# Kernel optimization log

Measured on AMD Instinct MI355X. Metric: run time of the kernel, lower is better.

The kernel has to match this reference:

```python
import jax, jax.numpy as jnp
import numpy as np

B, SEQ, D, INITIAL_D, T_DIFF = 256, 200, 256, 256, 1000


def _linear_params(key, fan_in, fan_out):
    k1, k2 = jax.random.split(key)
    lim = 1.0 / np.sqrt(fan_in)
    w = jax.random.uniform(k1, (fan_in, fan_out), minval=-lim, maxval=lim, dtype=jnp.float32)
    b = jax.random.uniform(k2, (fan_out,), minval=-lim, maxval=lim, dtype=jnp.float32)
    return w, b


def setup_inputs() -> dict:
    key = jax.random.key(0)
    ks = list(jax.random.split(key, 24))
    inp = {}
    inp["input_seqs"] = jax.random.normal(ks[0], (B, SEQ, INITIAL_D), dtype=jnp.float32)
    inp["masks"] = jnp.zeros((B, SEQ), dtype=jnp.int32)
    inp["lengths"] = jnp.full((B,), SEQ, dtype=jnp.int32)
    inp["seq_time_step"] = jax.random.uniform(ks[1], (B, SEQ), dtype=jnp.float32) * 360.0
    inp["code_masks"] = jnp.zeros((B, SEQ), dtype=jnp.int32)
    inp["diffusion_time_t"] = jax.random.randint(ks[2], (B,), 0, T_DIFF)
    inp["normal_noise"] = jax.random.normal(ks[3], (B, SEQ, D), dtype=jnp.float32)
    inp["predicted_noise"] = jax.random.normal(ks[4], (B, SEQ, D), dtype=jnp.float32) * 0.1
    inp["betas"] = jnp.linspace(1e-4, 0.02, T_DIFF, dtype=jnp.float32)
    names = [("emb2", INITIAL_D, D), ("Wall", D, 4 * D), ("Uall", D, 4 * D), ("Wd", D, D),
             ("time", 64, D), ("sel", 1, 64), ("whk", D, D), ("w1", 2 * D, 64),
             ("w2", 64, 2), ("out", D, 2)]
    for i, (nm, fi, fo) in enumerate(names):
        w, b = _linear_params(ks[5 + i], fi, fo)
        inp[nm + "_w"] = w
        inp[nm + "_b"] = b
    return inp


def reference(input_seqs, masks, lengths, seq_time_step, code_masks,
              diffusion_time_t, normal_noise, predicted_noise, betas,
              emb2_w, emb2_b, Wall_w, Wall_b, Uall_w, Uall_b, Wd_w, Wd_b,
              time_w, time_b, sel_w, sel_b, whk_w, whk_b,
              w1_w, w1_b, w2_w, w2_b, out_w, out_b):
    x = input_seqs @ emb2_w + emb2_b                      # [b,seq,d]  (initial_d != 0 path)
    b, seq, d = x.shape
    t = seq_time_step[..., None] / 180.0                  # [b,seq,1]
    tfeat = 1.0 - jnp.tanh(jnp.square(t @ sel_w + sel_b))  # [b,seq,64]
    time_feature = tfeat @ time_w + time_b                # [b,seq,d]

    def tlstm(xs_tmajor, tf_tmajor):
        # xs_tmajor, tf_tmajor: [seq, b, d] -> hidden states [b, seq, d]
        def step(carry, inp):
            h, c = carry
            xs, ts = inp
            c_s1 = jnp.tanh(c @ Wd_w + Wd_b)
            c_adj = c - c_s1 + c_s1 * ts                  # time-decayed cell
            gates = jax.nn.sigmoid(h @ Wall_w + Wall_b + xs @ Uall_w + Uall_b)
            f, i, o, ct = jnp.split(gates, 4, axis=-1)    # note: c_tmp uses sigmoid too
            c_new = f * c_adj + i * ct
            h_new = o * jnp.tanh(c_new)
            return (h_new, c_new), h_new
        zeros = jnp.zeros((xs_tmajor.shape[1], d), xs_tmajor.dtype)
        _, hs = jax.lax.scan(step, (zeros, zeros), (xs_tmajor, tf_tmajor))
        return hs.transpose(1, 0, 2)                      # [b,seq,d]

    tf_t = time_feature.transpose(1, 0, 2)
    outputs = tlstm(x.transpose(1, 0, 2), tf_t)

    # attention alignment (original always uses e_k = x[:, 0:1]) — fully vectorized over i>=1
    e_k = x[:, :1, :]                                     # [b,1,d]
    whk = outputs[:, :-1, :] @ whk_w + whk_b              # [b,seq-1,d]
    cat = jnp.concatenate([jnp.broadcast_to(e_k, whk.shape), whk], axis=-1)
    attn = jax.nn.softmax(jnp.tanh(cat @ w1_w + w1_b) @ w2_w + w2_b, axis=-1)  # [b,seq-1,2]
    aligned = jnp.concatenate([e_k, e_k * attn[..., 0:1] + whk * attn[..., 1:2]], axis=1)

    alpha = jnp.cumprod(1.0 - betas)[diffusion_time_t].reshape(-1, 1, 1)
    _noisy = aligned * jnp.sqrt(alpha) + normal_noise * jnp.sqrt(1.0 - alpha)  # UNet input (UNet output stubbed as predicted_noise)
    gen_x = aligned + (normal_noise - predicted_noise)
    gen_outputs = tlstm(gen_x.transpose(1, 0, 2), tf_t)

    out = jnp.max(outputs, axis=1) @ out_w + out_b        # max-pool over seq, then mlp
    gen_out = jnp.max(gen_outputs, axis=1) @ out_w + out_b
    return (out, gen_out, predicted_noise, normal_noise)
```

## Files before the change

### kernel.cpp

```cpp
#include <hip/hip_runtime.h>
#include <hip/hip_bf16.h>
#include <cstdint>

typedef __attribute__((ext_vector_type(8))) short short8;
typedef __attribute__((ext_vector_type(4))) float f32x4;
typedef unsigned short ushortT;

#define SEQ 200
#define NB  256

__device__ __forceinline__ float b2f(ushortT u){
    union { unsigned u; float f; } v; v.u = ((unsigned)u) << 16; return v.f;
}
__device__ __forceinline__ ushortT f2b(float f){
    union { float f; unsigned u; } v; v.f = f;
    unsigned r = v.u + 0x7FFFu + ((v.u >> 16) & 1u);
    return (ushortT)(r >> 16);
}
__device__ __forceinline__ float frcp(float x){
    float r; asm("v_rcp_f32 %0, %1" : "=v"(r) : "v"(x)); return r;
}
__device__ __forceinline__ float sigm(float x){ return frcp(1.0f + __expf(-x)); }
__device__ __forceinline__ float tanh_fast(float x){
    float ax = fabsf(x);
    float t = __expf(-2.0f * ax);
    float r = (1.0f - t) * frcp(1.0f + t);
    return copysignf(r, x);
}

__global__ void k_cvt(const float* __restrict__ in, ushortT* __restrict__ out){
    size_t i = ((size_t)blockIdx.x*256 + threadIdx.x)*4;
    float4 v = *(const float4*)(in + i);
    ushortT o[4] = { f2b(v.x), f2b(v.y), f2b(v.z), f2b(v.w) };
    *(int2*)(out + i) = *(int2*)o;
}

__global__ void k_swizzle(const float* __restrict__ src, int ncols,
                          ushortT* __restrict__ dst, int tile0){
    int Tl = blockIdx.x, q = blockIdx.y, l = threadIdx.x;
    int n  = Tl*16 + (l & 15);
    int kb = q*32 + (l >> 4)*8;
    short8 v;
    #pragma unroll
    for (int j = 0; j < 8; ++j) ((ushortT*)&v)[j] = f2b(src[(size_t)(kb + j)*ncols + n]);
    *(short8*)(dst + ((size_t)(tile0 + Tl)*8 + q)*512 + (size_t)l*8) = v;
}

__global__ void k_tft(const float* __restrict__ sts, const float* __restrict__ selw,
                      const float* __restrict__ selb, ushortT* __restrict__ tft){
    int l = threadIdx.x, g = blockIdx.x / SEQ, t = blockIdx.x % SEQ;
    int lm = l & 15, lq = l >> 4;
    float tv = sts[(size_t)(g*16 + lm)*SEQ + t] * (1.0f/180.0f);
    size_t base = (size_t)(g*SEQ + t)*1024 + (size_t)l*8;
    #pragma unroll
    for (int q = 0; q < 2; ++q){
        short8 v;
        #pragma unroll
        for (int j = 0; j < 8; ++j){
            int u = q*32 + lq*8 + j;
            float a = tv * selw[u] + selb[u];
            ((ushortT*)&v)[j] = f2b(1.0f - tanh_fast(a*a));
        }
        *(short8*)(tft + base + (size_t)q*512) = v;
    }
}

__global__ __launch_bounds__(512) void k_gemm256(const ushortT* A,
        const ushortT* __restrict__ Bswz, const float* __restrict__ bias, ushortT* out){
    __shared__ ushortT stage[16*256];
    int tid = threadIdx.x, w = tid >> 6, l = tid & 63, lm = l & 15, lq = l >> 4;
    size_t r0 = (size_t)blockIdx.x * 16;
    const f32x4 fz = {0.f,0.f,0.f,0.f};
    f32x4 acc[2] = {fz, fz};
    for (int q = 0; q < 8; ++q){
        short8 a = *(const short8*)(A + (r0 + lm)*256 + q*32 + lq*8);
        #pragma unroll
        for (int p = 0; p < 2; ++p){
            int T = 2*w + p;
            short8 b = *(const short8*)(Bswz + ((size_t)T*8 + q)*512 + (size_t)l*8);
            acc[p] = __builtin_amdgcn_mfma_f32_16x16x32_bf16(a, b, acc[p], 0, 0, 0);
        }
    }
    #pragma unroll
    for (int p = 0; p < 2; ++p){
        int n = (2*w + p)*16 + lm;
        float bs = bias[n];
        #pragma unroll
        for (int r = 0; r < 4; ++r)
            stage[(lq*4 + r)*256 + n] = f2b(acc[p][r] + bs);
    }
    __syncthreads();
    int row = tid >> 5, c8 = tid & 31;
    int4 v = *(const int4*)(stage + row*256 + c8*8);
    *(int4*)(out + (r0 + row)*256 + (size_t)c8*8) = v;
}

__global__ __launch_bounds__(256) void k_gemm64(const ushortT* __restrict__ A,
        const ushortT* __restrict__ Bswz, float* __restrict__ out){
    int tid = threadIdx.x, w = tid >> 6, l = tid & 63, lm = l & 15, lq = l >> 4;
    size_t r0 = (size_t)blockIdx.x * 16;
    const f32x4 fz = {0.f,0.f,0.f,0.f};
    f32x4 acc = fz;
    for (int q = 0; q < 8; ++q){
        short8 a = *(const short8*)(A + (r0 + lm)*256 + q*32 + lq*8);
        short8 b = *(const short8*)(Bswz + ((size_t)w*8 + q)*512 + (size_t)l*8);
        acc = __builtin_amdgcn_mfma_f32_16x16x32_bf16(a, b, acc, 0, 0, 0);
    }
    #pragma unroll
    for (int r = 0; r < 4; ++r)
        out[(r0 + lq*4 + r)*64 + w*16 + lm] = acc[r];
}

__global__ __launch_bounds__(512) void k_gemmgates(const ushortT* __restrict__ A,
        const ushortT* __restrict__ Bswz, const float* __restrict__ bW,
        const float* __restrict__ bU, ushortT* __restrict__ out){
    int tid = threadIdx.x, w = tid >> 6, l = tid & 63, lm = l & 15, lq = l >> 4;
    int g = blockIdx.x / SEQ, t = blockIdx.x % SEQ;
    const f32x4 fz = {0.f,0.f,0.f,0.f};
    f32x4 acc[8] = {fz,fz,fz,fz,fz,fz,fz,fz};
    const ushortT* Arow = A + ((size_t)(g*16 + lm)*SEQ + t)*256;
    for (int q = 0; q < 8; ++q){
        short8 a = *(const short8*)(Arow + q*32 + lq*8);
        #pragma unroll
        for (int gq = 0; gq < 4; ++gq)
        #pragma unroll
        for (int p = 0; p < 2; ++p){
            int T = gq*16 + 2*w + p;
            short8 b = *(const short8*)(Bswz + ((size_t)T*8 + q)*512 + (size_t)l*8);
            acc[gq*2+p] = __builtin_amdgcn_mfma_f32_16x16x32_bf16(a, b, acc[gq*2+p], 0, 0, 0);
        }
    }
    short8 ch[4];
    #pragma unroll
    for (int gq = 0; gq < 4; ++gq)
    #pragma unroll
    for (int p = 0; p < 2; ++p){
        int n = gq*256 + w*32 + p*16 + lm;
        float bs = bW[n] + bU[n];
        #pragma unroll
        for (int r = 0; r < 4; ++r)
            ((ushortT*)&ch[p*2 + (gq>>1)])[(gq&1)*4 + r] = f2b(acc[gq*2+p][r] + bs);
    }
    size_t base = (size_t)(g*SEQ + t)*16384 + (size_t)(w*64 + l)*32;
    #pragma unroll
    for (int ci = 0; ci < 4; ++ci) *(short8*)(out + base + ci*8) = ch[ci];
}

__global__ void k_zeroflags(unsigned* __restrict__ f){
    f[blockIdx.x*256 + threadIdx.x] = 0;
}

#define HB (16*264)
__global__ __launch_bounds__(512, 2) void k_scan(const ushortT* __restrict__ xg,
        const ushortT* __restrict__ tftg, const ushortT* __restrict__ Wswz,
        const ushortT* __restrict__ twswz, const float* __restrict__ wdb_g,
        const float* __restrict__ timeb, ushortT* __restrict__ hs,
        float* __restrict__ maxh, int write_hs,
        ushortT* __restrict__ xbuf, unsigned* __restrict__ flags, unsigned fb){
    extern __shared__ ushortT smem[];
    ushortT* wlds = smem + 4*HB;
    int tid = threadIdx.x, w = tid >> 6, l = tid & 63, lm = l & 15, lq = l >> 4;
    int blk = blockIdx.x;
    int h = blk >> 4, g = blk & 15;
    int pblk = (1 - h)*16 + g;
    int cw = h*8 + w;
    int col = cw*16 + lm;
    int l8 = l*8;
    float wdb = wdb_g[col];
    float tb  = timeb[col];
    short8 twf[2];
    #pragma unroll
    for (int q2 = 0; q2 < 2; ++q2)
        twf[q2] = *(const short8*)(twswz + ((size_t)cw*8 + q2)*512 + l8);
    short8 wg0[8], wg1[8], wg2[8], wdreg[8];
    #pragma unroll
    for (int q = 0; q < 8; ++q){
        wg0[q]   = *(const short8*)(Wswz + ((size_t)( 0 + cw)*8 + q)*512 + l8);
        wg1[q]   = *(const short8*)(Wswz + ((size_t)(16 + cw)*8 + q)*512 + l8);
        wg2[q]   = *(const short8*)(Wswz + ((size_t)(32 + cw)*8 + q)*512 + l8);
        wdreg[q] = *(const short8*)(Wswz + ((size_t)(64 + cw)*8 + q)*512 + l8);
    }
    float c[4], hm[4];
    #pragma unroll
    for (int i = 0; i < 4; ++i){ c[i] = 0.0f; hm[i] = -2.0f; }
    for (int i = tid; i < HB; i += 512){ smem[HB + i] = 0; smem[3*HB + i] = 0; }
    {
        const int4* wsrc = (const int4*)(Wswz + (size_t)(48 + h*8)*4096);
        int4* wdst = (int4*)wlds;
        for (int i = tid; i < 4096; i += 512) wdst[i] = wsrc[i];
    }
    __syncthreads();

    const ushortT* xg_g  = xg   + (size_t)g*SEQ*16384 + ((size_t)(cw>>1)*64 + l)*32 + (cw&1)*16;
    const ushortT* tft_g = tftg + (size_t)g*SEQ*1024  + (size_t)l8;
    const ushortT* wl    = wlds + (size_t)w*4096 + l8;
    const f32x4 fz = {0.f,0.f,0.f,0.f};

    for (int t = 0; t < SEQ; ++t){
        int pb = t & 1, ab = 1 - pb;
        const ushortT* hb = smem + (size_t)ab*HB;
        const ushortT* cb = smem + 2*HB + (size_t)ab*HB;
        short8 xA  = *(const short8*)(xg_g + (size_t)t*16384);
        short8 xB  = *(const short8*)(xg_g + (size_t)t*16384 + 8);
        short8 aT0 = *(const short8*)(tft_g + (size_t)t*1024);
        short8 aT1 = *(const short8*)(tft_g + (size_t)t*1024 + 512);

        f32x4 acc[5];
        #pragma unroll
        for (int i = 0; i < 5; ++i) acc[i] = fz;
        #pragma unroll
        for (int q = 0; q < 8; ++q){
            short8 a  = *(const short8*)(hb + lm*264 + q*32 + lq*8);
            short8 ca = *(const short8*)(cb + lm*264 + q*32 + lq*8);
            short8 b3 = *(const short8*)(wl + q*512);
            acc[0] = __builtin_amdgcn_mfma_f32_16x16x32_bf16(a,  wg0[q],   acc[0], 0, 0, 0);
            acc[1] = __builtin_amdgcn_mfma_f32_16x16x32_bf16(a,  wg1[q],   acc[1], 0, 0, 0);
            acc[2] = __builtin_amdgcn_mfma_f32_16x16x32_bf16(a,  wg2[q],   acc[2], 0, 0, 0);
            acc[3] = __builtin_amdgcn_mfma_f32_16x16x32_bf16(a,  b3,       acc[3], 0, 0, 0);
            acc[4] = __builtin_amdgcn_mfma_f32_16x16x32_bf16(ca, wdreg[q], acc[4], 0, 0, 0);
        }
        f32x4 acc_ts = fz;
        acc_ts = __builtin_amdgcn_mfma_f32_16x16x32_bf16(aT0, twf[0], acc_ts, 0, 0, 0);
        acc_ts = __builtin_amdgcn_mfma_f32_16x16x32_bf16(aT1, twf[1], acc_ts, 0, 0, 0);

        ushortT* hbw = smem + (size_t)pb*HB;
        ushortT* cbw = smem + 2*HB + (size_t)pb*HB;
        #pragma unroll
        for (int r = 0; r < 4; ++r){
            float F   = acc[0][r] + b2f(((const ushortT*)&xA)[r]);
            float I   = acc[1][r] + b2f(((const ushortT*)&xA)[4+r]);
            float O   = acc[2][r] + b2f(((const ushortT*)&xB)[r]);
            float CT  = acc[3][r] + b2f(((const ushortT*)&xB)[4+r]);
            float cwd = acc[4][r] + wdb;
            float ts  = acc_ts[r] + tb;
            float cc  = c[r];
            float cs1 = tanh_fast(cwd);
            float cadj = cc - cs1 + cs1*ts;
            float cn  = sigm(F)*cadj + sigm(I)*sigm(CT);
            float hv  = sigm(O)*tanh_fast(cn);
            c[r]  = cn;
            hm[r] = fmaxf(hm[r], hv);
            hbw[(lq*4 + r)*264 + col] = f2b(hv);
            cbw[(lq*4 + r)*264 + col] = f2b(cn);
        }
        __syncthreads();
        if (t < SEQ-1){
            {
                int part = tid >> 8, i = tid & 255, row = i >> 4, c16 = i & 15;
                const ushortT* src = (part ? cbw : hbw) + row*264 + h*128 + c16*8;
                union { int4 v; unsigned long long uu[2]; } u; u.v = *(const int4*)src;
                unsigned long long* dst = (unsigned long long*)(xbuf +
                    ((((size_t)blk*2 + pb)*2 + part)*16 + row)*128 + c16*8);
                __hip_atomic_store(dst+0, u.uu[0], __ATOMIC_RELAXED, __HIP_MEMORY_SCOPE_AGENT);
                __hip_atomic_store(dst+1, u.uu[1], __ATOMIC_RELAXED, __HIP_MEMORY_SCOPE_AGENT);
            }
            __syncthreads();
            if (tid == 0){
                __hip_atomic_store(&flags[(size_t)blk*64], fb + (unsigned)t + 1u,
                                   __ATOMIC_RELEASE, __HIP_MEMORY_SCOPE_AGENT);
                unsigned want = fb + (unsigned)t + 1u;
                for (int it = 0; it < 20000000; ++it){
                    if (__hip_atomic_load(&flags[(size_t)pblk*64],
                            __ATOMIC_ACQUIRE, __HIP_MEMORY_SCOPE_AGENT) >= want) break;
                    __builtin_amdgcn_s_sleep(2);
                }
            }
            if (write_hs && tid >= 256){
                int i = tid - 256, row = i >> 4, c16 = i & 15;
                int4 v = *(const int4*)(hbw + row*264 + h*128 + c16*8);
                *(int4*)(hs + ((size_t)(g*16 + row)*SEQ + t)*256 + h*128 + c16*8) = v;
            }
            __syncthreads();
            {
                int part = tid >> 8, i = tid & 255, row = i >> 4, c16 = i & 15;
                const unsigned long long* src = (const unsigned long long*)(xbuf +
                    ((((size_t)pblk*2 + pb)*2 + part)*16 + row)*128 + c16*8);
                unsigned long long u0 = __hip_atomic_load(src+0, __ATOMIC_RELAXED, __HIP_MEMORY_SCOPE_AGENT);
                unsigned long long u1 = __hip_atomic_load(src+1, __ATOMIC_RELAXED, __HIP_MEMORY_SCOPE_AGENT);
                ushortT* dst = (part ? cbw : hbw) + row*264 + (1-h)*128 + c16*8;
                union { int4 v; unsigned long long uu[2]; } u;
                u.uu[0] = u0; u.uu[1] = u1;
                *(int4*)dst = u.v;
            }
            __syncthreads();
        } else {
            if (write_hs && tid < 256){
                int row = tid >> 4, c16 = tid & 15;
                int4 v = *(const int4*)(hbw + row*264 + h*128 + c16*8);
                *(int4*)(hs + ((size_t)(g*16 + row)*SEQ + t)*256 + h*128 + c16*8) = v;
            }
        }
    }
    #pragma unroll
    for (int r = 0; r < 4; ++r)
        maxh[(size_t)(g*16 + lq*4 + r)*256 + col] = hm[r];
}

__global__ void k_ekcopy(const ushortT* __restrict__ x, ushortT* __restrict__ ek){
    int b = blockIdx.x, l = threadIdx.x;
    ((int2*)(ek + (size_t)b*256))[l] = ((const int2*)(x + (size_t)b*SEQ*256))[l];
}

__global__ void k_ekw(const ushortT* __restrict__ ek, const float* __restrict__ w1w,
                      const float* __restrict__ w1b, float* __restrict__ ekw){
    int b = blockIdx.x, l = threadIdx.x;
    float acc = w1b[l];
    const ushortT* e = ek + (size_t)b*256;
    for (int d = 0; d < 256; ++d)
        acc += b2f(e[d]) * w1w[(size_t)d*64 + l];
    ekw[b*64 + l] = acc;
}

__global__ __launch_bounds__(512) void k_attn(const ushortT* __restrict__ ekbuf,
        const ushortT* __restrict__ whk, const float* __restrict__ ekw,
        const float* __restrict__ w1p, const float* __restrict__ w2w,
        const float* __restrict__ w2b, const float* __restrict__ nn,
        const float* __restrict__ pn, ushortT* __restrict__ genx){
    int w = threadIdx.x >> 6, l = threadIdx.x & 63;
    int wid = blockIdx.x*8 + w;
    int b = wid / SEQ, sp = wid % SEQ;
    const ushortT* ek = ekbuf + (size_t)b*256;
    const ushortT* wr = whk + ((size_t)b*SEQ + (sp > 0 ? sp-1 : 0))*256;
    size_t orow = ((size_t)b*SEQ + sp)*256;
    float a0, a1;
    if (sp == 0){ a0 = 1.0f; a1 = 0.0f; }
    else {
        float acc = ekw[b*64 + l] + w1p[((size_t)b*SEQ + sp-1)*64 + l];
        float u  = tanh_fast(acc);
        float p0 = u * w2w[l*2 + 0];
        float p1 = u * w2w[l*2 + 1];
        #pragma unroll
        for (int off = 32; off >= 1; off >>= 1){
            p0 += __shfl_xor(p0, off, 64);
            p1 += __shfl_xor(p1, off, 64);
        }
        float v0 = p0 + w2b[0], v1 = p1 + w2b[1];
        a0 = sigm(v0 - v1); a1 = 1.0f - a0;
    }
    #pragma unroll
    for (int i = 0; i < 4; ++i){
        int d = i*64 + l;
        float al = b2f(ek[d])*a0 + b2f(wr[d])*a1;
        float gv = al + nn[orow + d] - pn[orow + d];
        genx[orow + d] = f2b(gv);
    }
}

__global__ void k_final(const float* __restrict__ mh1, const float* __restrict__ mh2,
                        const float* __restrict__ ow, const float* __restrict__ ob,
                        float* __restrict__ outp){
    int th = threadIdx.x;
    const float* mh = blockIdx.x ? mh2 : mh1;
    int b = th >> 1, cc = th & 1;
    float acc = ob[cc];
    for (int d = 0; d < 256; ++d)
        acc += mh[b*256 + d] * ow[d*2 + cc];
    outp[blockIdx.x*512 + th] = acc;
}

extern "C" void kernel_launch(void* const* d_in, const int* in_sizes, int n_in,
                              void* d_out, int out_size, void* d_ws, size_t ws_size,
                              hipStream_t stream) {
    const float* input_seqs = (const float*)d_in[0];
    const float* seq_time   = (const float*)d_in[3];
    const float* nn     = (const float*)d_in[6];
    const float* pn     = (const float*)d_in[7];
    const float* emb2_w = (const float*)d_in[9];
    const float* emb2_b = (const float*)d_in[10];
    const float* Wall_w = (const float*)d_in[11];
    const float* Wall_b = (const float*)d_in[12];
    const float* Uall_w = (const float*)d_in[13];
    const float* Uall_b = (const float*)d_in[14];
    const float* Wd_w   = (const float*)d_in[15];
    const float* Wd_b   = (const float*)d_in[16];
    const float* time_w = (const float*)d_in[17];
    const float* time_b = (const float*)d_in[18];
    const float* sel_w  = (const float*)d_in[19];
    const float* sel_b  = (const float*)d_in[20];
    const float* whk_w  = (const float*)d_in[21];
    const float* whk_b  = (const float*)d_in[22];
    const float* w1_w   = (const float*)d_in[23];
    const float* w1_b   = (const float*)d_in[24];
    const float* w2_w   = (const float*)d_in[25];
    const float* w2_b   = (const float*)d_in[26];
    const float* out_w  = (const float*)d_in[27];
    const float* out_b  = (const float*)d_in[28];

    const size_t NSZ = (size_t)in_sizes[6];

    static bool attr_done = false;
    if (!attr_done){
        hipFuncSetAttribute((const void*)k_scan,
                            hipFuncAttributeMaxDynamicSharedMemorySize, 160*1024);
        attr_done = true;
    }
    const size_t SCAN_LDS = (size_t)(4*HB + 8*4096) * sizeof(ushortT);

    char* wsb = (char*)d_ws;
    size_t off = 0;
    auto alloc = [&](size_t bytes){ void* p = wsb + off; off += (bytes + 255) & ~(size_t)255; return p; };
    ushortT* Wswz  = (ushortT*)alloc(80u*8*512*2);
    ushortT* Uswz  = (ushortT*)alloc(64u*8*512*2);
    ushortT* Eswz  = (ushortT*)alloc(16u*8*512*2);
    ushortT* Hswz  = (ushortT*)alloc(16u*8*512*2);
    ushortT* TWswz = (ushortT*)alloc(16u*8*512*2);
    ushortT* W1swz = (ushortT*)alloc(4u*8*512*2);
    ushortT* TFT   = (ushortT*)alloc((size_t)16*SEQ*1024*2);
    ushortT* X     = (ushortT*)alloc((size_t)NB*SEQ*256*2);
    ushortT* XG    = (ushortT*)alloc((size_t)16*SEQ*16384*2);
    ushortT* HS    = (ushortT*)alloc((size_t)NB*SEQ*256*2);
    ushortT* EK    = (ushortT*)alloc((size_t)NB*256*2);
    float*  MAXH1  = (float*)alloc((size_t)NB*256*4);
    float*  MAXH2  = (float*)alloc((size_t)NB*256*4);
    float*  EKW    = (float*)alloc((size_t)NB*64*4);
    float*  W1P    = (float*)alloc((size_t)NB*SEQ*64*4);
    ushortT* XBUF  = (ushortT*)alloc((size_t)32*2*2*16*128*2);
    unsigned* FLAGS= (unsigned*)alloc((size_t)32*64*4);

    float* outp = (float*)d_out;
    hipMemcpyAsync(outp + 1024,       pn, NSZ*4, hipMemcpyDeviceToDevice, stream);
    hipMemcpyAsync(outp + 1024 + NSZ, nn, NSZ*4, hipMemcpyDeviceToDevice, stream);

    k_zeroflags<<<8, 256, 0, stream>>>(FLAGS);
    k_swizzle<<<dim3(64,8), 64, 0, stream>>>(Wall_w, 1024, Wswz, 0);
    k_swizzle<<<dim3(16,8), 64, 0, stream>>>(Wd_w,    256, Wswz, 64);
    k_swizzle<<<dim3(64,8), 64, 0, stream>>>(Uall_w, 1024, Uswz, 0);
    k_swizzle<<<dim3(16,8), 64, 0, stream>>>(emb2_w,  256, Eswz, 0);
    k_swizzle<<<dim3(16,8), 64, 0, stream>>>(whk_w,   256, Hswz, 0);
    k_swizzle<<<dim3(16,2), 64, 0, stream>>>(time_w,  256, TWswz, 0);
    k_swizzle<<<dim3(4,8),  64, 0, stream>>>(w1_w + 256*64, 64, W1swz, 0);

    k_tft<<<3200, 64, 0, stream>>>(seq_time, sel_w, sel_b, TFT);
    k_cvt<<<12800, 256, 0, stream>>>(input_seqs, HS);
    k_gemm256<<<3200, 512, 0, stream>>>(HS, Eswz, emb2_b, X);
    k_ekcopy<<<256, 64, 0, stream>>>(X, EK);
    k_ekw<<<256, 64, 0, stream>>>(EK, w1_w, w1_b, EKW);
    k_gemmgates<<<3200, 512, 0, stream>>>(X, Uswz, Wall_b, Uall_b, XG);
    k_scan<<<32, 512, SCAN_LDS, stream>>>(XG, TFT, Wswz, TWswz, Wd_b, time_b, HS, MAXH1, 1,
                                          XBUF, FLAGS, 0u);
    k_gemm256<<<3200, 512, 0, stream>>>(HS, Hswz, whk_b, HS);
    k_gemm64<<<3200, 256, 0, stream>>>(HS, W1swz, W1P);
    k_attn<<<6400, 512, 0, stream>>>(EK, HS, EKW, W1P, w2_w, w2_b, nn, pn, X);
    k_gemmgates<<<3200, 512, 0, stream>>>(X, Uswz, Wall_b, Uall_b, XG);
    k_scan<<<32, 512, SCAN_LDS, stream>>>(XG, TFT, Wswz, TWswz, Wd_b, time_b, HS, MAXH2, 0,
                                          XBUF, FLAGS, (unsigned)SEQ);
    k_final<<<2, 512, 0, stream>>>(MAXH1, MAXH2, out_w, out_b, outp);
}
```

Before: 2.116 ms.

## Restructure LSTM scan exchange: per-wave flag sync, register-loaded peer halves, local-first MFMA

The recurrent scan now keeps only the block's own half of h/c in LDS and loads the partner block's half straight from the global exchange buffer into MFMA fragment registers. The K-loop is reordered so the local half is processed first, with the remote half's MFMAs issued after the time-feature MFMAs. Each wave now signals with an atomic counter (8 increments per step) and spins on its own, replacing two block-wide barriers and the single-thread handshake. The Wd weights move from registers to swizzled LDS, and next-step gate inputs are prefetched. In exchange the kernel uses more LDS and does more atomic flag traffic, and the flag base offset for the second scan changes to match the new counting.

```diff
diff --git a/kernel.cpp b/kernel.cpp
--- a/kernel.cpp
+++ b/kernel.cpp
@@ -26,6 +26,13 @@
     float t = __expf(-2.0f * ax);
     float r = (1.0f - t) * frcp(1.0f + t);
     return copysignf(r, x);
+}
+__device__ __forceinline__ short8 ld_frag16(const ushortT* p){
+    const unsigned long long* s = (const unsigned long long*)p;
+    union { short8 v; unsigned long long u[2]; } r;
+    r.u[0] = __hip_atomic_load(s+0, __ATOMIC_RELAXED, __HIP_MEMORY_SCOPE_AGENT);
+    r.u[1] = __hip_atomic_load(s+1, __ATOMIC_RELAXED, __HIP_MEMORY_SCOPE_AGENT);
+    return r.v;
 }
 
 __global__ void k_cvt(const float* __restrict__ in, ushortT* __restrict__ out){
@@ -150,81 +157,125 @@
     f[blockIdx.x*256 + threadIdx.x] = 0;
 }
 
-#define HB (16*264)
+#define SL  132
+#define HCL (16*SL)
 __global__ __launch_bounds__(512, 2) void k_scan(const ushortT* __restrict__ xg,
         const ushortT* __restrict__ tftg, const ushortT* __restrict__ Wswz,
         const ushortT* __restrict__ twswz, const float* __restrict__ wdb_g,
         const float* __restrict__ timeb, ushortT* __restrict__ hs,
         float* __restrict__ maxh, int write_hs,
-        ushortT* __restrict__ xbuf, unsigned* __restrict__ flags, unsigned fb){
+        ushortT* __restrict__ xbuf, unsigned* __restrict__ flags, unsigned fb8){
     extern __shared__ ushortT smem[];
-    ushortT* wlds = smem + 4*HB;
+    ushortT* wl3b = smem + 4*HCL;
+    ushortT* wlDb = smem + 4*HCL + 32768;
     int tid = threadIdx.x, w = tid >> 6, l = tid & 63, lm = l & 15, lq = l >> 4;
     int blk = blockIdx.x;
     int h = blk >> 4, g = blk & 15;
     int pblk = (1 - h)*16 + g;
     int cw = h*8 + w;
     int col = cw*16 + lm;
-    int l8 = l*8;
+    int l8 = l*8, h4 = h*4;
     float wdb = wdb_g[col];
     float tb  = timeb[col];
     short8 twf[2];
     #pragma unroll
     for (int q2 = 0; q2 < 2; ++q2)
         twf[q2] = *(const short8*)(twswz + ((size_t)cw*8 + q2)*512 + l8);
-    short8 wg0[8], wg1[8], wg2[8], wdreg[8];
-    #pragma unroll
-    for (int q = 0; q < 8; ++q){
-        wg0[q]   = *(const short8*)(Wswz + ((size_t)( 0 + cw)*8 + q)*512 + l8);
-        wg1[q]   = *(const short8*)(Wswz + ((size_t)(16 + cw)*8 + q)*512 + l8);
-        wg2[q]   = *(const short8*)(Wswz + ((size_t)(32 + cw)*8 + q)*512 + l8);
-        wdreg[q] = *(const short8*)(Wswz + ((size_t)(64 + cw)*8 + q)*512 + l8);
+    short8 wg0[8], wg1[8], wg2[8];
+    #pragma unroll
+    for (int s = 0; s < 8; ++s){
+        int q = s ^ h4;
+        wg0[s] = *(const short8*)(Wswz + ((size_t)( 0 + cw)*8 + q)*512 + l8);
+        wg1[s] = *(const short8*)(Wswz + ((size_t)(16 + cw)*8 + q)*512 + l8);
+        wg2[s] = *(const short8*)(Wswz + ((size_t)(32 + cw)*8 + q)*512 + l8);
     }
     float c[4], hm[4];
     #pragma unroll
     for (int i = 0; i < 4; ++i){ c[i] = 0.0f; hm[i] = -2.0f; }
-    for (int i = tid; i < HB; i += 512){ smem[HB + i] = 0; smem[3*HB + i] = 0; }
+    for (int i = tid; i < HCL; i += 512){ smem[HCL + i] = 0; smem[3*HCL + i] = 0; }
     {
-        const int4* wsrc = (const int4*)(Wswz + (size_t)(48 + h*8)*4096);
-        int4* wdst = (int4*)wlds;
-        for (int i = tid; i < 4096; i += 512) wdst[i] = wsrc[i];
+        const int4* s3 = (const int4*)(Wswz + (size_t)(48 + h*8)*4096);
+        const int4* sD = (const int4*)(Wswz + (size_t)(64 + h*8)*4096);
+        int4* d3 = (int4*)wl3b;
+        int4* dD = (int4*)wlDb;
+        for (int i = tid; i < 4096; i += 512){
+            int qc = (i >> 6) & 7, rest = i & ~(7 << 6);
+            int j = rest | ((qc ^ h4) << 6);
+            d3[j] = s3[i];
+            dD[j] = sD[i];
+        }
     }
     __syncthreads();
 
     const ushortT* xg_g  = xg   + (size_t)g*SEQ*16384 + ((size_t)(cw>>1)*64 + l)*32 + (cw&1)*16;
     const ushortT* tft_g = tftg + (size_t)g*SEQ*1024  + (size_t)l8;
-    const ushortT* wl    = wlds + (size_t)w*4096 + l8;
+    const ushortT* wl3   = wl3b + (size_t)w*4096 + l8;
+    const ushortT* wlD   = wlDb + (size_t)w*4096 + l8;
     const f32x4 fz = {0.f,0.f,0.f,0.f};
+    const short8 sz = {0,0,0,0,0,0,0,0};
+    short8 ra0=sz, ra1=sz, ra2=sz, ra3=sz, rc0=sz, rc1=sz, rc2=sz, rc3=sz;
+    short8 xA = *(const short8*)(xg_g);
+    short8 xB = *(const short8*)(xg_g + 8);
 
     for (int t = 0; t < SEQ; ++t){
         int pb = t & 1, ab = 1 - pb;
-        const ushortT* hb = smem + (size_t)ab*HB;
-        const ushortT* cb = smem + 2*HB + (size_t)ab*HB;
-        short8 xA  = *(const short8*)(xg_g + (size_t)t*16384);
-        short8 xB  = *(const short8*)(xg_g + (size_t)t*16384 + 8);
+        const ushortT* hbL = smem + (size_t)ab*HCL;
+        const ushortT* cbL = smem + 2*HCL + (size_t)ab*HCL;
         short8 aT0 = *(const short8*)(tft_g + (size_t)t*1024);
         short8 aT1 = *(const short8*)(tft_g + (size_t)t*1024 + 512);
+        size_t tn = (size_t)(t+1 < SEQ ? t+1 : t);
+        short8 nxA = *(const short8*)(xg_g + tn*16384);
+        short8 nxB = *(const short8*)(xg_g + tn*16384 + 8);
 
         f32x4 acc[5];
         #pragma unroll
         for (int i = 0; i < 5; ++i) acc[i] = fz;
         #pragma unroll
-        for (int q = 0; q < 8; ++q){
-            short8 a  = *(const short8*)(hb + lm*264 + q*32 + lq*8);
-            short8 ca = *(const short8*)(cb + lm*264 + q*32 + lq*8);
-            short8 b3 = *(const short8*)(wl + q*512);
-            acc[0] = __builtin_amdgcn_mfma_f32_16x16x32_bf16(a,  wg0[q],   acc[0], 0, 0, 0);
-            acc[1] = __builtin_amdgcn_mfma_f32_16x16x32_bf16(a,  wg1[q],   acc[1], 0, 0, 0);
-            acc[2] = __builtin_amdgcn_mfma_f32_16x16x32_bf16(a,  wg2[q],   acc[2], 0, 0, 0);
-            acc[3] = __builtin_amdgcn_mfma_f32_16x16x32_bf16(a,  b3,       acc[3], 0, 0, 0);
-            acc[4] = __builtin_amdgcn_mfma_f32_16x16x32_bf16(ca, wdreg[q], acc[4], 0, 0, 0);
+        for (int s = 0; s < 4; ++s){
+            short8 a  = *(const short8*)(hbL + lm*SL + s*32 + lq*8);
+            short8 ca = *(const short8*)(cbL + lm*SL + s*32 + lq*8);
+            short8 b3 = *(const short8*)(wl3 + s*512);
+            short8 bd = *(const short8*)(wlD + s*512);
+            acc[0] = __builtin_amdgcn_mfma_f32_16x16x32_bf16(a,  wg0[s], acc[0], 0, 0, 0);
+            acc[1] = __builtin_amdgcn_mfma_f32_16x16x32_bf16(a,  wg1[s], acc[1], 0, 0, 0);
+            acc[2] = __builtin_amdgcn_mfma_f32_16x16x32_bf16(a,  wg2[s], acc[2], 0, 0, 0);
+            acc[3] = __builtin_amdgcn_mfma_f32_16x16x32_bf16(a,  b3,     acc[3], 0, 0, 0);
+            acc[4] = __builtin_amdgcn_mfma_f32_16x16x32_bf16(ca, bd,     acc[4], 0, 0, 0);
         }
         f32x4 acc_ts = fz;
         acc_ts = __builtin_amdgcn_mfma_f32_16x16x32_bf16(aT0, twf[0], acc_ts, 0, 0, 0);
         acc_ts = __builtin_amdgcn_mfma_f32_16x16x32_bf16(aT1, twf[1], acc_ts, 0, 0, 0);
-
-        ushortT* hbw = smem + (size_t)pb*HB;
-        ushortT* cbw = smem + 2*HB + (size_t)pb*HB;
+        {
+            short8 b3, bd;
+            b3 = *(const short8*)(wl3 + 4*512); bd = *(const short8*)(wlD + 4*512);
+            acc[0] = __builtin_amdgcn_mfma_f32_16x16x32_bf16(ra0, wg0[4], acc[0], 0, 0, 0);
+            acc[1] = __builtin_amdgcn_mfma_f32_16x16x32_bf16(ra0, wg1[4], acc[1], 0, 0, 0);
+            acc[2] = __builtin_amdgcn_mfma_f32_16x16x32_bf16(ra0, wg2[4], acc[2], 0, 0, 0);
+            acc[3] = __builtin_amdgcn_mfma_f32_16x16x32_bf16(ra0, b3,     acc[3], 0, 0, 0);
+            acc[4] = __builtin_amdgcn_mfma_f32_16x16x32_bf16(rc0, bd,     acc[4], 0, 0, 0);
+            b3 = *(const short8*)(wl3 + 5*512); bd = *(const short8*)(wlD + 5*512);
+            acc[0] = __builtin_amdgcn_mfma_f32_16x16x32_bf16(ra1, wg0[5], acc[0], 0, 0, 0);
+            acc[1] = __builtin_amdgcn_mfma_f32_16x16x32_bf16(ra1, wg1[5], acc[1], 0, 0, 0);
+            acc[2] = __builtin_amdgcn_mfma_f32_16x16x32_bf16(ra1, wg2[5], acc[2], 0, 0, 0);
+            acc[3] = __builtin_amdgcn_mfma_f32_16x16x32_bf16(ra1, b3,     acc[3], 0, 0, 0);
+            acc[4] = __builtin_amdgcn_mfma_f32_16x16x32_bf16(rc1, bd,     acc[4], 0, 0, 0);
+            b3 = *(const short8*)(wl3 + 6*512); bd = *(const short8*)(wlD + 6*512);
+            acc[0] = __builtin_amdgcn_mfma_f32_16x16x32_bf16(ra2, wg0[6], acc[0], 0, 0, 0);
+            acc[1] = __builtin_amdgcn_mfma_f32_16x16x32_bf16(ra2, wg1[6], acc[1], 0, 0, 0);
+            acc[2] = __builtin_amdgcn_mfma_f32_16x16x32_bf16(ra2, wg2[6], acc[2], 0, 0, 0);
+            acc[3] = __builtin_amdgcn_mfma_f32_16x16x32_bf16(ra2, b3,     acc[3], 0, 0, 0);
+            acc[4] = __builtin_amdgcn_mfma_f32_16x16x32_bf16(rc2, bd,     acc[4], 0, 0, 0);
+            b3 = *(const short8*)(wl3 + 7*512); bd = *(const short8*)(wlD + 7*512);
+            acc[0] = __builtin_amdgcn_mfma_f32_16x16x32_bf16(ra3, wg0[7], acc[0], 0, 0, 0);
+            acc[1] = __builtin_amdgcn_mfma_f32_16x16x32_bf16(ra3, wg1[7], acc[1], 0, 0, 0);
+            acc[2] = __builtin_amdgcn_mfma_f32_16x16x32_bf16(ra3, wg2[7], acc[2], 0, 0, 0);
+            acc[3] = __builtin_amdgcn_mfma_f32_16x16x32_bf16(ra3, b3,     acc[3], 0, 0, 0);
+            acc[4] = __builtin_amdgcn_mfma_f32_16x16x32_bf16(rc3, bd,     acc[4], 0, 0, 0);
+        }
+
+        ushortT* hbw = smem + (size_t)pb*HCL;
+        ushortT* cbw = smem + 2*HCL + (size_t)pb*HCL;
+        int colL = w*16 + lm;
         #pragma unroll
         for (int r = 0; r < 4; ++r){
             float F   = acc[0][r] + b2f(((const ushortT*)&xA)[r]);
@@ -240,56 +291,45 @@
             float hv  = sigm(O)*tanh_fast(cn);
             c[r]  = cn;
             hm[r] = fmaxf(hm[r], hv);
-            hbw[(lq*4 + r)*264 + col] = f2b(hv);
-            cbw[(lq*4 + r)*264 + col] = f2b(cn);
+            hbw[(lq*4 + r)*SL + colL] = f2b(hv);
+            cbw[(lq*4 + r)*SL + colL] = f2b(cn);
         }
         __syncthreads();
         if (t < SEQ-1){
-            {
-                int part = tid >> 8, i = tid & 255, row = i >> 4, c16 = i & 15;
-                const ushortT* src = (part ? cbw : hbw) + row*264 + h*128 + c16*8;
-                union { int4 v; unsigned long long uu[2]; } u; u.v = *(const int4*)src;
-                unsigned long long* dst = (unsigned long long*)(xbuf +
-                    ((((size_t)blk*2 + pb)*2 + part)*16 + row)*128 + c16*8);
-                __hip_atomic_store(dst+0, u.uu[0], __ATOMIC_RELAXED, __HIP_MEMORY_SCOPE_AGENT);
-                __hip_atomic_store(dst+1, u.uu[1], __ATOMIC_RELAXED, __HIP_MEMORY_SCOPE_AGENT);
+            int part = tid >> 8, i = tid & 255, row = i >> 4, c16 = i & 15;
+            const ushortT* src = (part ? cbw : hbw) + row*SL + c16*8;
+            union { int4 v; unsigned long long uu[2]; } u; u.v = *(const int4*)src;
+            unsigned long long* dst = (unsigned long long*)(xbuf +
+                ((((size_t)blk*2 + pb)*2 + part)*16 + row)*128 + c16*8);
+            __hip_atomic_store(dst+0, u.uu[0], __ATOMIC_RELAXED, __HIP_MEMORY_SCOPE_AGENT);
+            __hip_atomic_store(dst+1, u.uu[1], __ATOMIC_RELAXED, __HIP_MEMORY_SCOPE_AGENT);
+            if (write_hs && !part)
+                *(int4*)(hs + ((size_t)(g*16 + row)*SEQ + t)*256 + h*128 + c16*8) = u.v;
+            if (l == 0)
+                __hip_atomic_fetch_add(&flags[(size_t)blk*64], 1u,
+                                       __ATOMIC_RELEASE, __HIP_MEMORY_SCOPE_AGENT);
+            unsigned want = fb8 + 8u*(unsigned)(t+1);
+            unsigned v = 0;
+            for (int it = 0; it < 20000000; ++it){
+                if (l == 0)
+                    v = __hip_atomic_load(&flags[(size_t)pblk*64],
+                                          __ATOMIC_ACQUIRE, __HIP_MEMORY_SCOPE_AGENT);
+                v = __shfl(v, 0, 64);
+                if (v >= want) break;
+                __builtin_amdgcn_s_sleep(1);
             }
-            __syncthreads();
-            if (tid == 0){
-                __hip_atomic_store(&flags[(size_t)blk*64], fb + (unsigned)t + 1u,
-                                   __ATOMIC_RELEASE, __HIP_MEMORY_SCOPE_AGENT);
-                unsigned want = fb + (unsigned)t + 1u;
-                for (int it = 0; it < 20000000; ++it){
-                    if (__hip_atomic_load(&flags[(size_t)pblk*64],
-                            __ATOMIC_ACQUIRE, __HIP_MEMORY_SCOPE_AGENT) >= want) break;
-                    __builtin_amdgcn_s_sleep(2);
-                }
-            }
-            if (write_hs && tid >= 256){
-                int i = tid - 256, row = i >> 4, c16 = i & 15;
-                int4 v = *(const int4*)(hbw + row*264 + h*128 + c16*8);
-                *(int4*)(hs + ((size_t)(g*16 + row)*SEQ + t)*256 + h*128 + c16*8) = v;
-            }
-            __syncthreads();
-            {
-                int part = tid >> 8, i = tid & 255, row = i >> 4, c16 = i & 15;
-                const unsigned long long* src = (const unsigned long long*)(xbuf +
-                    ((((size_t)pblk*2 + pb)*2 + part)*16 + row)*128 + c16*8);
-                unsigned long long u0 = __hip_atomic_load(src+0, __ATOMIC_RELAXED, __HIP_MEMORY_SCOPE_AGENT);
-                unsigned long long u1 = __hip_atomic_load(src+1, __ATOMIC_RELAXED, __HIP_MEMORY_SCOPE_AGENT);
-                ushortT* dst = (part ? cbw : hbw) + row*264 + (1-h)*128 + c16*8;
-                union { int4 v; unsigned long long uu[2]; } u;
-                u.uu[0] = u0; u.uu[1] = u1;
-                *(int4*)dst = u.v;
-            }
-            __syncthreads();
-        } else {
-            if (write_hs && tid < 256){
-                int row = tid >> 4, c16 = tid & 15;
-                int4 v = *(const int4*)(hbw + row*264 + h*128 + c16*8);
-                *(int4*)(hs + ((size_t)(g*16 + row)*SEQ + t)*256 + h*128 + c16*8) = v;
-            }
-        }
+            const ushortT* hsrc = xbuf + ((((size_t)pblk*2 + pb)*2 + 0)*16 + lm)*128 + lq*8;
+            const ushortT* csrc = xbuf + ((((size_t)pblk*2 + pb)*2 + 1)*16 + lm)*128 + lq*8;
+            ra0 = ld_frag16(hsrc +  0); ra1 = ld_frag16(hsrc + 32);
+            ra2 = ld_frag16(hsrc + 64); ra3 = ld_frag16(hsrc + 96);
+            rc0 = ld_frag16(csrc +  0); rc1 = ld_frag16(csrc + 32);
+            rc2 = ld_frag16(csrc + 64); rc3 = ld_frag16(csrc + 96);
+        } else if (write_hs && tid < 256){
+            int row = tid >> 4, c16 = tid & 15;
+            int4 v = *(const int4*)(hbw + row*SL + c16*8);
+            *(int4*)(hs + ((size_t)(g*16 + row)*SEQ + t)*256 + h*128 + c16*8) = v;
+        }
+        xA = nxA; xB = nxB;
     }
     #pragma unroll
     for (int r = 0; r < 4; ++r)
@@ -394,7 +434,7 @@
                             hipFuncAttributeMaxDynamicSharedMemorySize, 160*1024);
         attr_done = true;
     }
-    const size_t SCAN_LDS = (size_t)(4*HB + 8*4096) * sizeof(ushortT);
+    const size_t SCAN_LDS = (size_t)(4*HCL + 2*32768) * sizeof(ushortT);
 
     char* wsb = (char*)d_ws;
     size_t off = 0;
@@ -443,6 +483,6 @@
     k_attn<<<6400, 512, 0, stream>>>(EK, HS, EKW, W1P, w2_w, w2_b, nn, pn, X);
     k_gemmgates<<<3200, 512, 0, stream>>>(X, Uswz, Wall_b, Uall_b, XG);
     k_scan<<<32, 512, SCAN_LDS, stream>>>(XG, TFT, Wswz, TWswz, Wd_b, time_b, HS, MAXH2, 0,
-                                          XBUF, FLAGS, (unsigned)SEQ);
+                                          XBUF, FLAGS, 8u*(SEQ-1));
     k_final<<<2, 512, 0, stream>>>(MAXH1, MAXH2, out_w, out_b, outp);
 }
```

After: 4.673 ms. +120.8%, slower.
